# Kernel tuning notes

Measured on AMD Instinct MI355X. Metric: run time of the kernel, lower is better.

## Reference

```python
import jax, jax.numpy as jnp
import numpy as np
from jax import lax

T, B, A_DIM, Z_DIM, K_MIX, HID = 128, 256, 16, 32, 8, 128
Q_REG = 1e-3
R_REG = 1e-3


def setup_inputs() -> dict:
    key = jax.random.key(0)
    ks = jax.random.split(key, 16)
    s = 1.0 / np.sqrt(HID)
    reg = 0.9
    as_ = jax.random.normal(ks[0], (T, B, A_DIM), dtype=jnp.float32)
    mat_A_K = (1.0 - reg) * jax.random.normal(ks[1], (K_MIX, Z_DIM, Z_DIM)) + reg * jnp.eye(Z_DIM)
    mat_C_K = (1.0 - reg) * jax.random.normal(ks[2], (K_MIX, A_DIM, Z_DIM)) + reg * jnp.eye(A_DIM, Z_DIM)
    # Cholesky factors of near-identity SPD matrices (as in torch init)
    Q_L = jnp.tril(0.05 * jax.random.normal(ks[3], (Z_DIM, Z_DIM))) + jnp.eye(Z_DIM)
    R_L = jnp.tril(0.05 * jax.random.normal(ks[4], (A_DIM, A_DIM))) + jnp.eye(A_DIM)
    init_mean = jnp.zeros((Z_DIM,), dtype=jnp.float32)
    init_cov = jnp.eye(Z_DIM, dtype=jnp.float32)
    u = lambda k, shp: jax.random.uniform(k, shp, minval=-s, maxval=s, dtype=jnp.float32)
    return dict(
        as_=as_, mat_A_K=mat_A_K, mat_C_K=mat_C_K, Q_L=Q_L, R_L=R_L,
        init_mean=init_mean, init_cov=init_cov,
        W_ih0=u(ks[5], (4 * HID, A_DIM)), W_hh0=u(ks[6], (4 * HID, HID)),
        b_ih0=u(ks[7], (4 * HID,)), b_hh0=u(ks[8], (4 * HID,)),
        W_ih1=u(ks[9], (4 * HID, HID)), W_hh1=u(ks[10], (4 * HID, HID)),
        b_ih1=u(ks[11], (4 * HID,)), b_hh1=u(ks[12], (4 * HID,)),
        W_out=u(ks[13], (K_MIX, HID)), b_out=u(ks[14], (K_MIX,)),
    )


def _lstm_cell(x, h, c, W_ih, W_hh, b_ih, b_hh):
    g = x @ W_ih.T + b_ih + h @ W_hh.T + b_hh
    i, f, gg, o = jnp.split(g, 4, axis=-1)
    c2 = jax.nn.sigmoid(f) * c + jax.nn.sigmoid(i) * jnp.tanh(gg)
    h2 = jax.nn.sigmoid(o) * jnp.tanh(c2)
    return h2, c2


def reference(as_, mat_A_K, mat_C_K, Q_L, R_L, init_mean, init_cov,
              W_ih0, W_hh0, b_ih0, b_hh0, W_ih1, W_hh1, b_ih1, b_hh1,
              W_out, b_out):
    Tn, Bn, a_dim = as_.shape
    Kn, z_dim, _ = mat_A_K.shape
    Hn = W_hh0.shape[1]
    Q = Q_L @ Q_L.T + Q_REG * jnp.eye(z_dim, dtype=as_.dtype)
    R = R_L @ R_L.T + R_REG * jnp.eye(a_dim, dtype=as_.dtype)

    def weight_model(a, h0, c0, h1, c1):
        h0, c0 = _lstm_cell(a, h0, c0, W_ih0, W_hh0, b_ih0, b_hh0)
        h1, c1 = _lstm_cell(h0, h1, c1, W_ih1, W_hh1, b_ih1, b_hh1)
        w = jax.nn.softmax(h1 @ W_out.T + b_out, axis=-1)
        return w, h0, c0, h1, c1

    def step(carry, a_t):
        mean_p, cov_p, weight, h0, c0, h1, c1 = carry
        # mixture matrices for this step (weight == previous step's w_next; ones at t=0)
        mat_A = jnp.einsum('bk,kij->bij', weight, mat_A_K)
        mat_C = jnp.einsum('bk,kij->bij', weight, mat_C_K)
        # sample_control = ('mean','mean'), observation_mask=None -> a = as_[t]
        w_next, h0, c0, h1, c1 = weight_model(a_t, h0, c0, h1, c1)
        mat_A_next = jnp.einsum('bk,kij->bij', w_next, mat_A_K)
        CP = mat_C @ cov_p                                   # (B,a,z)
        S = CP @ jnp.swapaxes(mat_C, 1, 2) + R               # (B,a,a)
        K_t = cov_p @ jnp.swapaxes(mat_C, 1, 2) @ jnp.linalg.inv(S)
        mean_t = mean_p + K_t @ (a_t[..., None] - mat_C @ mean_p)
        mean_p2 = mat_A_next @ mean_t
        cov_t = cov_p - K_t @ CP
        cov_t = 0.5 * (cov_t + jnp.swapaxes(cov_t, 1, 2))
        cov_p2 = mat_A_next @ cov_t @ jnp.swapaxes(mat_A_next, 1, 2) + Q
        cov_p2 = 0.5 * (cov_p2 + jnp.swapaxes(cov_p2, 1, 2))
        new_carry = (mean_p2, cov_p2, w_next, h0, c0, h1, c1)
        outs = (mean_t, cov_t, mean_p2, cov_p2, mat_A, mat_C, a_t)
        return new_carry, outs

    init = (
        jnp.broadcast_to(init_mean[None, :, None], (Bn, z_dim, 1)),
        jnp.broadcast_to(init_cov[None], (Bn, z_dim, z_dim)),
        jnp.ones((Bn, Kn), dtype=as_.dtype),
        jnp.zeros((Bn, Hn), dtype=as_.dtype), jnp.zeros((Bn, Hn), dtype=as_.dtype),
        jnp.zeros((Bn, Hn), dtype=as_.dtype), jnp.zeros((Bn, Hn), dtype=as_.dtype),
    )
    carry, ys = lax.scan(step, init, as_)
    means, covs, next_means, next_covs, mat_As, mat_Cs, a_seq = ys
    w_fin = carry[2]
    mat_A_fin = jnp.einsum('bk,kij->bij', w_fin, mat_A_K)
    mat_C_fin = jnp.einsum('bk,kij->bij', w_fin, mat_C_K)
    mat_As = jnp.concatenate([mat_As, mat_A_fin[None]], axis=0)   # (T+1,B,z,z)
    mat_Cs = jnp.concatenate([mat_Cs, mat_C_fin[None]], axis=0)   # (T+1,B,a,z)
    a_out = a_seq[:, None]                                        # (T,1,B,a) as in torch stack
    return means, covs, next_means, next_covs, mat_As, mat_Cs, a_out
```

## Files before the change

### kernel.cpp

```cpp
#include <hip/hip_runtime.h>
#include <hip/hip_fp16.h>
#include <math.h>

#define T_STEPS 128
#define B_SZ 256
#define AD 16
#define ZD 32
#define KM 8
#define HID 128
#define G4H 512
#define NTHR 512

#define WS_WQ   0
#define WS_WI0  98304
#define WS_BS0  102400
#define WS_BS1  102912
#define WS_Q    103424
#define WS_R    104448

typedef float f32x4 __attribute__((ext_vector_type(4)));

__device__ __forceinline__ unsigned pk16(float lo, float hi) {
  unsigned a = __half_as_ushort(__float2half_rn(lo));
  unsigned b = __half_as_ushort(__float2half_rn(hi));
  return a | (b << 16);
}

__global__ void ssm_prep_kernel(const float* __restrict__ Wih0, const float* __restrict__ Whh0,
                                const float* __restrict__ Wih1, const float* __restrict__ Whh1,
                                const float* __restrict__ bih0, const float* __restrict__ bhh0,
                                const float* __restrict__ bih1, const float* __restrict__ bhh1,
                                const float* __restrict__ QL, const float* __restrict__ RL,
                                float* __restrict__ ws) {
  unsigned* wsu = (unsigned*)ws;
  int tid = blockIdx.x * blockDim.x + threadIdx.x;
  int nt = gridDim.x * blockDim.x;
  for (int j = tid; j < G4H; j += nt) {
    for (int d4 = 0; d4 < 48; ++d4) {
      for (int m = 0; m < 4; ++m) {
        int dd = (d4 & 15) * 4 + m;
        const float* src = (d4 < 16) ? Whh0 : (d4 < 32) ? Wih1 : Whh1;
        wsu[WS_WQ + (d4 * 512 + j) * 4 + m] =
            pk16(src[j * 128 + 2 * dd], src[j * 128 + 2 * dd + 1]);
      }
    }
    for (int k = 0; k < 8; ++k)
      wsu[WS_WI0 + k * 512 + j] = pk16(Wih0[j * 16 + 2 * k], Wih0[j * 16 + 2 * k + 1]);
    ws[WS_BS0 + j] = bih0[j] + bhh0[j];
    ws[WS_BS1 + j] = bih1[j] + bhh1[j];
  }
  for (int e = tid; e < ZD * ZD; e += nt) {
    int i = e >> 5, j = e & 31;
    float s = 0.f;
    for (int k = 0; k < ZD; ++k) s += QL[i * ZD + k] * QL[j * ZD + k];
    if (i == j) s += 0.001f;
    ws[WS_Q + e] = s;
  }
  for (int e = tid; e < AD * AD; e += nt) {
    int i = e >> 4, j = e & 15;
    float s = 0.f;
    for (int k = 0; k < AD; ++k) s += RL[i * AD + k] * RL[j * AD + k];
    if (i == j) s += 0.001f;
    ws[WS_R + e] = s;
  }
}

__device__ __forceinline__ float sigm(float x) { return 1.0f / (1.0f + expf(-x)); }
__device__ __forceinline__ float dotv(f32x4 a, f32x4 b) {
  return a[0] * b[0] + a[1] * b[1] + a[2] * b[2] + a[3] * b[3];
}
__device__ __forceinline__ void st_nt(float* p, float v) { __builtin_nontemporal_store(v, p); }
__device__ __forceinline__ void st_nt4(float* p, f32x4 v) {
  __builtin_nontemporal_store(v, (f32x4*)p);
}

__device__ __forceinline__ float dot2f(unsigned a, unsigned b, float c) {
#if __has_builtin(__builtin_amdgcn_fdot2)
  typedef _Float16 h2 __attribute__((ext_vector_type(2)));
  union U { unsigned u; h2 h; };
  U ua, ub; ua.u = a; ub.u = b;
  return __builtin_amdgcn_fdot2(ua.h, ub.h, c, false);
#else
  union U { unsigned u; _Float16 h[2]; };
  U ua, ub; ua.u = a; ub.u = b;
  return c + (float)ua.h[0] * (float)ub.h[0] + (float)ua.h[1] * (float)ub.h[1];
#endif
}

struct alignas(16) LS {
  unsigned ap[8];
  unsigned h0p[64];
  unsigned h1p[64];
  float g[G4H];
  float lgp[16];
};

__global__ void __launch_bounds__(NTHR, 2) ssm_lstm_kernel(
    const float* __restrict__ as_, const float* __restrict__ AK, const float* __restrict__ CK,
    const float* __restrict__ Wout, const float* __restrict__ bout,
    const float* __restrict__ ws, float* __restrict__ out) {
  __shared__ LS s;
  const int tid = threadIdx.x;
  const int b = blockIdx.x;
  const unsigned* wsu = (const unsigned*)ws;
  const uint4* Wg = (const uint4*)(wsu + WS_WQ);
  const f32x4* AK4 = (const f32x4*)AK;
  const f32x4* CK4 = (const f32x4*)CK;

  float* o_As = out + (size_t)T_STEPS * B_SZ * ZD + (size_t)T_STEPS * B_SZ * ZD * ZD +
                (size_t)T_STEPS * B_SZ * ZD + (size_t)T_STEPS * B_SZ * ZD * ZD;
  float* o_Cs = o_As + (size_t)(T_STEPS + 1) * B_SZ * ZD * ZD;
  float* o_a = o_Cs + (size_t)(T_STEPS + 1) * B_SZ * AD * ZD;

  const uint4* h0p4 = (const uint4*)s.h0p;
  const uint4* h1p4 = (const uint4*)s.h1p;
  const uint4* ap4 = (const uint4*)s.ap;

  unsigned wi0r[8];
  #pragma unroll
  for (int k = 0; k < 8; ++k) wi0r[k] = wsu[WS_WI0 + k * 512 + tid];
  const float bs0r = ws[WS_BS0 + tid];
  const float bs1r = ws[WS_BS1 + tid];
  float woutr[8];
  #pragma unroll
  for (int gi = 0; gi < KM; ++gi) woutr[gi] = (tid < HID) ? Wout[gi * HID + tid] : 0.f;
  float boutr[8];
  #pragma unroll
  for (int k = 0; k < KM; ++k) boutr[k] = bout[k];

  float c0r = 0.f, c1r = 0.f;

  if (tid < 64) { s.h0p[tid] = 0u; s.h1p[tid] = 0u; }
  if (tid < AD) {
    float v = as_[(size_t)b * AD + tid];
    ((__half*)s.ap)[tid] = __float2half_rn(v);
    st_nt(&o_a[(size_t)b * AD + tid], v);
  }
  if (tid < 256) {
    f32x4 acc = {0.f, 0.f, 0.f, 0.f};
    #pragma unroll
    for (int k = 0; k < KM; ++k) acc += AK4[k * 256 + tid];
    st_nt4(&o_As[(size_t)b * 1024 + tid * 4], acc);
  } else if (tid < 384) {
    int idx = tid - 256;
    f32x4 acc = {0.f, 0.f, 0.f, 0.f};
    #pragma unroll
    for (int k = 0; k < KM; ++k) acc += CK4[k * 128 + idx];
    st_nt4(&o_Cs[(size_t)b * 512 + idx * 4], acc);
  }
  __syncthreads();

  for (int t = 0; t < T_STEPS; ++t) {
    const size_t tb2 = (size_t)(t + 1) * B_SZ + b;

    {
      float acc = bs0r;
      #pragma unroll
      for (int k4 = 0; k4 < 2; ++k4) {
        uint4 av = ap4[k4];
        acc = dot2f(av.x, wi0r[k4 * 4 + 0], acc);
        acc = dot2f(av.y, wi0r[k4 * 4 + 1], acc);
        acc = dot2f(av.z, wi0r[k4 * 4 + 2], acc);
        acc = dot2f(av.w, wi0r[k4 * 4 + 3], acc);
      }
      #pragma unroll
      for (int d4 = 0; d4 < 16; ++d4) {
        uint4 w = Wg[d4 * 512 + tid];
        uint4 hv = h0p4[d4];
        acc = dot2f(hv.x, w.x, acc);
        acc = dot2f(hv.y, w.y, acc);
        acc = dot2f(hv.z, w.z, acc);
        acc = dot2f(hv.w, w.w, acc);
      }
      s.g[tid] = acc;
    }
    __syncthreads();

    if (tid < HID) {
      float ig = sigm(s.g[tid]);
      float fg = sigm(s.g[HID + tid]);
      float gg = tanhf(s.g[2 * HID + tid]);
      float og = sigm(s.g[3 * HID + tid]);
      c0r = fg * c0r + ig * gg;
      ((__half*)s.h0p)[tid] = __float2half_rn(og * tanhf(c0r));
    }
    __syncthreads();

    {
      float acc = bs1r;
      #pragma unroll
      for (int d4 = 0; d4 < 16; ++d4) {
        uint4 w = Wg[(16 + d4) * 512 + tid];
        uint4 hv = h0p4[d4];
        acc = dot2f(hv.x, w.x, acc);
        acc = dot2f(hv.y, w.y, acc);
        acc = dot2f(hv.z, w.z, acc);
        acc = dot2f(hv.w, w.w, acc);
      }
      #pragma unroll
      for (int d4 = 0; d4 < 16; ++d4) {
        uint4 w = Wg[(32 + d4) * 512 + tid];
        uint4 hv = h1p4[d4];
        acc = dot2f(hv.x, w.x, acc);
        acc = dot2f(hv.y, w.y, acc);
        acc = dot2f(hv.z, w.z, acc);
        acc = dot2f(hv.w, w.w, acc);
      }
      s.g[tid] = acc;
    }
    __syncthreads();

    if (tid < HID) {
      float ig = sigm(s.g[tid]);
      float fg = sigm(s.g[HID + tid]);
      float gg = tanhf(s.g[2 * HID + tid]);
      float og = sigm(s.g[3 * HID + tid]);
      c1r = fg * c1r + ig * gg;
      float h1u = og * tanhf(c1r);
      ((__half*)s.h1p)[tid] = __float2half_rn(h1u);
      int w2 = tid >> 6, lane = tid & 63;
      #pragma unroll
      for (int gi = 0; gi < KM; ++gi) {
        float p = woutr[gi] * h1u;
        #pragma unroll
        for (int m = 32; m >= 1; m >>= 1) p += __shfl_xor(p, m);
        if (lane == 0) s.lgp[w2 * KM + gi] = p;
      }
    }
    __syncthreads();

    {
      float lg[KM];
      float mx = -1e30f;
      #pragma unroll
      for (int k = 0; k < KM; ++k) {
        lg[k] = s.lgp[k] + s.lgp[KM + k] + boutr[k];
        mx = fmaxf(mx, lg[k]);
      }
      float sum = 0.f;
      #pragma unroll
      for (int k = 0; k < KM; ++k) { lg[k] = expf(lg[k] - mx); sum += lg[k]; }
      float inv = 1.0f / sum;
      #pragma unroll
      for (int k = 0; k < KM; ++k) lg[k] *= inv;
      if (tid < 256) {
        f32x4 acc = {0.f, 0.f, 0.f, 0.f};
        #pragma unroll
        for (int k = 0; k < KM; ++k) acc += lg[k] * AK4[k * 256 + tid];
        st_nt4(&o_As[tb2 * 1024 + tid * 4], acc);
      } else if (tid < 384) {
        int idx = tid - 256;
        f32x4 acc = {0.f, 0.f, 0.f, 0.f};
        #pragma unroll
        for (int k = 0; k < KM; ++k) acc += lg[k] * CK4[k * 128 + idx];
        st_nt4(&o_Cs[tb2 * 512 + idx * 4], acc);
      } else if (tid >= 448 && tid < 448 + AD && t < T_STEPS - 1) {
        int i = tid - 448;
        float v = as_[tb2 * AD + i];
        ((__half*)s.ap)[i] = __float2half_rn(v);
        st_nt(&o_a[tb2 * AD + i], v);
      }
    }
    __syncthreads();
  }
}

struct alignas(16) KS {
  float P[ZD * 36];
  float An[ZD * 36];
  float Mt[ZD * 36];
  float MtT[ZD * 36];
  float Sy[ZD * 36];
  float ACt[ZD * 36];
  float Qs[ZD * 36];
  float C[AD * 36];
  float Aug[AD * 52];
  float Kk[ZD * 20];
  float Rs[AD * AD];
  float meanp[ZD], meant[ZD], r[AD], af[AD];
};

__global__ void __launch_bounds__(256, 1) ssm_kalman_kernel(
    const float* __restrict__ as_, const float* __restrict__ initm,
    const float* __restrict__ initc, const float* __restrict__ ws,
    float* __restrict__ out) {
  __shared__ KS s;
  const int l = threadIdx.x;
  const int b = blockIdx.x;
  const int i32 = l & 31, cq = l >> 5;
  const int i16 = l & 15, j16 = l >> 4;

  float* o_means = out;
  float* o_covs = o_means + (size_t)T_STEPS * B_SZ * ZD;
  float* o_nmean = o_covs + (size_t)T_STEPS * B_SZ * ZD * ZD;
  float* o_ncovs = o_nmean + (size_t)T_STEPS * B_SZ * ZD;
  const float* o_As = o_ncovs + (size_t)T_STEPS * B_SZ * ZD * ZD;
  const float* o_Cs = o_As + (size_t)(T_STEPS + 1) * B_SZ * ZD * ZD;

  f32x4* P4 = (f32x4*)s.P;
  f32x4* An4 = (f32x4*)s.An;
  f32x4* Mt4 = (f32x4*)s.Mt;
  f32x4* MtT4 = (f32x4*)s.MtT;
  f32x4* Sy4 = (f32x4*)s.Sy;
  f32x4* ACt4 = (f32x4*)s.ACt;
  f32x4* Q4 = (f32x4*)s.Qs;
  f32x4* C4 = (f32x4*)s.C;
  f32x4* Aug4 = (f32x4*)s.Aug;
  f32x4* Kk4 = (f32x4*)s.Kk;
  f32x4* af4 = (f32x4*)s.af;
  const f32x4* r4 = (const f32x4*)s.r;
  const f32x4* meanp4 = (const f32x4*)s.meanp;
  const f32x4* meant4 = (const f32x4*)s.meant;

  #pragma unroll
  for (int q = 0; q < 4; ++q) {
    int e = q * 256 + l;
    s.P[(e >> 5) * 36 + (e & 31)] = initc[e];
    s.Qs[(e >> 5) * 36 + (e & 31)] = ws[WS_Q + e];
  }
  s.Rs[l] = ws[WS_R + l];
  if (l < ZD) s.meanp[l] = initm[l];
  {
    const f32x4* gc = (const f32x4*)&o_Cs[(size_t)b * 512];
    if (l < 128) C4[(l >> 3) * 9 + (l & 7)] = gc[l];
    const f32x4* ga = (const f32x4*)&o_As[((size_t)B_SZ + b) * 1024];
    An4[(l >> 3) * 9 + (l & 7)] = ga[l];
    if (l < 4) af4[l] = ((const f32x4*)&as_[(size_t)b * AD])[l];
  }
  __syncthreads();

  for (int t = 0; t < T_STEPS; ++t) {
    const size_t tb = (size_t)t * B_SZ + b;
    const bool pf = (t < T_STEPS - 1);

    f32x4 pfC = {0, 0, 0, 0};
    f32x4 pfA = {0, 0, 0, 0};
    f32x4 pfa = {0, 0, 0, 0};
    if (pf) {
      if (l >= 128) pfC = ((const f32x4*)&o_Cs[(tb + B_SZ) * 512])[l - 128];
      pfA = ((const f32x4*)&o_As[(tb + 2 * B_SZ) * 1024])[l];
      if (l < 4) pfa = ((const f32x4*)&as_[(tb + B_SZ) * AD])[l];
    }

    {
      float a0 = 0.f, a1 = 0.f;
      #pragma unroll
      for (int k4 = 0; k4 < 8; ++k4) {
        f32x4 cr = C4[i16 * 9 + k4];
        a0 += dotv(cr, P4[j16 * 9 + k4]);
        a1 += dotv(cr, P4[(j16 + 16) * 9 + k4]);
      }
      s.Aug[i16 * 52 + AD + j16] = a0;
      s.Aug[i16 * 52 + AD + j16 + 16] = a1;
    }
    __syncthreads();

    {
      float acc = s.Rs[i16 * AD + j16];
      #pragma unroll
      for (int k4 = 0; k4 < 8; ++k4)
        acc += dotv(Aug4[i16 * 13 + 4 + k4], C4[j16 * 9 + k4]);
      s.Aug[i16 * 52 + j16] = acc;
      if (l >= 240) {
        int ii = l - 240;
        float rr = s.af[ii];
        #pragma unroll
        for (int k4 = 0; k4 < 8; ++k4) rr -= dotv(C4[ii * 9 + k4], meanp4[k4]);
        s.r[ii] = rr;
      }
    }
    __syncthreads();

    if (l < 64) {
      const int lc = (l < 48) ? l : 47;
      float col[16];
      #pragma unroll
      for (int i = 0; i < AD; ++i) col[i] = s.Aug[i * 52 + lc];
      #pragma unroll
      for (int j = 0; j < AD; ++j) {
        float pd = __shfl(col[j], j);
        float pinv = 1.0f / pd;
        float oldj = col[j];
        #pragma unroll
        for (int i = 0; i < AD; ++i) {
          if (i == j) continue;
          float fi = __shfl(col[i], j);
          col[i] = fmaf(-(fi * pinv), oldj, col[i]);
        }
        col[j] = oldj * pinv;
      }
      if (l >= AD && l < AD + ZD) {
        int rr = l - AD;
        f32x4 v0 = {col[0], col[1], col[2], col[3]};
        f32x4 v1 = {col[4], col[5], col[6], col[7]};
        f32x4 v2 = {col[8], col[9], col[10], col[11]};
        f32x4 v3 = {col[12], col[13], col[14], col[15]};
        Kk4[rr * 5 + 0] = v0;
        Kk4[rr * 5 + 1] = v1;
        Kk4[rr * 5 + 2] = v2;
        Kk4[rr * 5 + 3] = v3;
      }
    } else if (pf && l >= 128) {
      int idx = l - 128;
      C4[(idx >> 3) * 9 + (idx & 7)] = pfC;
    }
    __syncthreads();

    {
      f32x4 acc = {0.f, 0.f, 0.f, 0.f};
      #pragma unroll
      for (int k4 = 0; k4 < 4; ++k4) {
        f32x4 kv = Kk4[i32 * 5 + k4];
        #pragma unroll
        for (int kk = 0; kk < 4; ++kk) {
          f32x4 cpk = Aug4[(4 * k4 + kk) * 13 + 4 + cq];
          acc += kv[kk] * cpk;
        }
      }
      f32x4 mv = P4[i32 * 9 + cq] - acc;
      Mt4[i32 * 9 + cq] = mv;
      #pragma unroll
      for (int jj = 0; jj < 4; ++jj) s.MtT[(4 * cq + jj) * 36 + i32] = mv[jj];
    }
    __syncthreads();

    {
      f32x4 sv = 0.5f * (Mt4[i32 * 9 + cq] + MtT4[i32 * 9 + cq]);
      Sy4[i32 * 9 + cq] = sv;
      st_nt4(&o_covs[tb * 1024 + i32 * 32 + cq * 4], sv);
      if (l < ZD) {
        float acc = s.meanp[l];
        #pragma unroll
        for (int m = 0; m < 4; ++m) acc += dotv(Kk4[l * 5 + m], r4[m]);
        s.meant[l] = acc;
        st_nt(&o_means[tb * ZD + l], acc);
      }
    }
    __syncthreads();

    {
      float c0 = 0.f, c1 = 0.f, c2 = 0.f, c3 = 0.f;
      #pragma unroll
      for (int k4 = 0; k4 < 8; ++k4) {
        f32x4 an = An4[i32 * 9 + k4];
        c0 += dotv(an, Sy4[(4 * cq + 0) * 9 + k4]);
        c1 += dotv(an, Sy4[(4 * cq + 1) * 9 + k4]);
        c2 += dotv(an, Sy4[(4 * cq + 2) * 9 + k4]);
        c3 += dotv(an, Sy4[(4 * cq + 3) * 9 + k4]);
      }
      f32x4 v = {c0, c1, c2, c3};
      ACt4[i32 * 9 + cq] = v;
    }
    __syncthreads();

    {
      if (l < ZD) {
        float acc = 0.f;
        #pragma unroll
        for (int k4 = 0; k4 < 8; ++k4) acc += dotv(An4[l * 9 + k4], meant4[k4]);
        s.meanp[l] = acc;
        st_nt(&o_nmean[tb * ZD + l], acc);
      }
      float c0 = 0.f, c1 = 0.f, c2 = 0.f, c3 = 0.f;
      #pragma unroll
      for (int k4 = 0; k4 < 8; ++k4) {
        f32x4 ac = ACt4[i32 * 9 + k4];
        c0 += dotv(ac, An4[(4 * cq + 0) * 9 + k4]);
        c1 += dotv(ac, An4[(4 * cq + 1) * 9 + k4]);
        c2 += dotv(ac, An4[(4 * cq + 2) * 9 + k4]);
        c3 += dotv(ac, An4[(4 * cq + 3) * 9 + k4]);
      }
      f32x4 mv = {c0, c1, c2, c3};
      Mt4[i32 * 9 + cq] = mv;
      #pragma unroll
      for (int jj = 0; jj < 4; ++jj) s.MtT[(4 * cq + jj) * 36 + i32] = mv[jj];
    }
    __syncthreads();

    {
      f32x4 pv = 0.5f * (Mt4[i32 * 9 + cq] + MtT4[i32 * 9 + cq]) + Q4[i32 * 9 + cq];
      P4[i32 * 9 + cq] = pv;
      st_nt4(&o_ncovs[tb * 1024 + i32 * 32 + cq * 4], pv);
    }
    __syncthreads();

    if (pf) {
      An4[(l >> 3) * 9 + (l & 7)] = pfA;
      if (l < 4) af4[l] = pfa;
    }
    __syncthreads();
  }
}

extern "C" void kernel_launch(void* const* d_in, const int* in_sizes, int n_in,
                              void* d_out, int out_size, void* d_ws, size_t ws_size,
                              hipStream_t stream) {
  const float* as_ = (const float*)d_in[0];
  const float* AK = (const float*)d_in[1];
  const float* CK = (const float*)d_in[2];
  const float* QL = (const float*)d_in[3];
  const float* RL = (const float*)d_in[4];
  const float* initm = (const float*)d_in[5];
  const float* initc = (const float*)d_in[6];
  const float* Wih0 = (const float*)d_in[7];
  const float* Whh0 = (const float*)d_in[8];
  const float* bih0 = (const float*)d_in[9];
  const float* bhh0 = (const float*)d_in[10];
  const float* Wih1 = (const float*)d_in[11];
  const float* Whh1 = (const float*)d_in[12];
  const float* bih1 = (const float*)d_in[13];
  const float* bhh1 = (const float*)d_in[14];
  const float* Wout = (const float*)d_in[15];
  const float* bout = (const float*)d_in[16];
  float* ws = (float*)d_ws;
  float* out = (float*)d_out;

  ssm_prep_kernel<<<16, 256, 0, stream>>>(Wih0, Whh0, Wih1, Whh1, bih0, bhh0, bih1, bhh1,
                                          QL, RL, ws);
  ssm_lstm_kernel<<<B_SZ, NTHR, 0, stream>>>(as_, AK, CK, Wout, bout, ws, out);
  ssm_kalman_kernel<<<B_SZ, 256, 0, stream>>>(as_, initm, initc, ws, out);
}
```

Baseline: 1.588 ms.

## Process two batch rows per LSTM block and merge Kalman output stores into one phase

The LSTM kernel now handles two batch elements per workgroup, so each weight fragment loaded from global memory feeds two dot-product accumulators. This halves weight traffic per row and halves the grid to 128 blocks. The catch is that fewer blocks run on the GPU, which has 256 CUs. The Kalman kernel also defers its means, covs and next-mean stores to the final phase and folds the prefetch update into it, removing one barrier per step.

```diff
diff --git a/kernel.cpp b/kernel.cpp
--- a/kernel.cpp
+++ b/kernel.cpp
@@ -9,7 +9,6 @@
 #define KM 8
 #define HID 128
 #define G4H 512
-#define NTHR 512
 
 #define WS_WQ   0
 #define WS_WI0  98304
@@ -88,20 +87,20 @@
 }
 
 struct alignas(16) LS {
-  unsigned ap[8];
-  unsigned h0p[64];
-  unsigned h1p[64];
-  float g[G4H];
-  float lgp[16];
+  unsigned ap[2][8];
+  unsigned h0p[2][64];
+  unsigned h1p[2][64];
+  float g[2][G4H];
+  float lgp[4][KM];
 };
 
-__global__ void __launch_bounds__(NTHR, 2) ssm_lstm_kernel(
+__global__ void __launch_bounds__(512, 2) ssm_lstm_kernel(
     const float* __restrict__ as_, const float* __restrict__ AK, const float* __restrict__ CK,
     const float* __restrict__ Wout, const float* __restrict__ bout,
     const float* __restrict__ ws, float* __restrict__ out) {
   __shared__ LS s;
   const int tid = threadIdx.x;
-  const int b = blockIdx.x;
+  const int b0 = blockIdx.x * 2;
   const unsigned* wsu = (const unsigned*)ws;
   const uint4* Wg = (const uint4*)(wsu + WS_WQ);
   const f32x4* AK4 = (const f32x4*)AK;
@@ -112,9 +111,12 @@
   float* o_Cs = o_As + (size_t)(T_STEPS + 1) * B_SZ * ZD * ZD;
   float* o_a = o_Cs + (size_t)(T_STEPS + 1) * B_SZ * AD * ZD;
 
-  const uint4* h0p4 = (const uint4*)s.h0p;
-  const uint4* h1p4 = (const uint4*)s.h1p;
-  const uint4* ap4 = (const uint4*)s.ap;
+  const uint4* ap40 = (const uint4*)s.ap[0];
+  const uint4* ap41 = (const uint4*)s.ap[1];
+  const uint4* h0p40 = (const uint4*)s.h0p[0];
+  const uint4* h0p41 = (const uint4*)s.h0p[1];
+  const uint4* h1p40 = (const uint4*)s.h1p[0];
+  const uint4* h1p41 = (const uint4*)s.h1p[1];
 
   unsigned wi0r[8];
   #pragma unroll
@@ -123,142 +125,162 @@
   const float bs1r = ws[WS_BS1 + tid];
   float woutr[8];
   #pragma unroll
-  for (int gi = 0; gi < KM; ++gi) woutr[gi] = (tid < HID) ? Wout[gi * HID + tid] : 0.f;
+  for (int gi = 0; gi < KM; ++gi)
+    woutr[gi] = (tid < 256) ? Wout[gi * HID + (tid & 127)] : 0.f;
   float boutr[8];
   #pragma unroll
   for (int k = 0; k < KM; ++k) boutr[k] = bout[k];
 
   float c0r = 0.f, c1r = 0.f;
 
-  if (tid < 64) { s.h0p[tid] = 0u; s.h1p[tid] = 0u; }
-  if (tid < AD) {
-    float v = as_[(size_t)b * AD + tid];
-    ((__half*)s.ap)[tid] = __float2half_rn(v);
-    st_nt(&o_a[(size_t)b * AD + tid], v);
-  }
-  if (tid < 256) {
+  if (tid < 128) { ((unsigned*)s.h0p)[tid] = 0u; ((unsigned*)s.h1p)[tid] = 0u; }
+  if (tid < 32) {
+    int bq = tid >> 4, i = tid & 15;
+    float v = as_[(size_t)(b0 + bq) * AD + i];
+    ((__half*)s.ap[bq])[i] = __float2half_rn(v);
+    st_nt(&o_a[(size_t)(b0 + bq) * AD + i], v);
+  }
+  {
+    int bq = tid >> 8, e = tid & 255;
     f32x4 acc = {0.f, 0.f, 0.f, 0.f};
     #pragma unroll
-    for (int k = 0; k < KM; ++k) acc += AK4[k * 256 + tid];
-    st_nt4(&o_As[(size_t)b * 1024 + tid * 4], acc);
-  } else if (tid < 384) {
-    int idx = tid - 256;
+    for (int k = 0; k < KM; ++k) acc += AK4[k * 256 + e];
+    st_nt4(&o_As[((size_t)(b0 + bq)) * 1024 + e * 4], acc);
+  }
+  if (tid < 256) {
+    int bq = tid >> 7, e = tid & 127;
     f32x4 acc = {0.f, 0.f, 0.f, 0.f};
     #pragma unroll
-    for (int k = 0; k < KM; ++k) acc += CK4[k * 128 + idx];
-    st_nt4(&o_Cs[(size_t)b * 512 + idx * 4], acc);
+    for (int k = 0; k < KM; ++k) acc += CK4[k * 128 + e];
+    st_nt4(&o_Cs[((size_t)(b0 + bq)) * 512 + e * 4], acc);
   }
   __syncthreads();
 
   for (int t = 0; t < T_STEPS; ++t) {
-    const size_t tb2 = (size_t)(t + 1) * B_SZ + b;
-
-    {
-      float acc = bs0r;
+    {
+      float a0 = bs0r, a1 = bs0r;
       #pragma unroll
       for (int k4 = 0; k4 < 2; ++k4) {
-        uint4 av = ap4[k4];
-        acc = dot2f(av.x, wi0r[k4 * 4 + 0], acc);
-        acc = dot2f(av.y, wi0r[k4 * 4 + 1], acc);
-        acc = dot2f(av.z, wi0r[k4 * 4 + 2], acc);
-        acc = dot2f(av.w, wi0r[k4 * 4 + 3], acc);
+        uint4 av0 = ap40[k4], av1 = ap41[k4];
+        a0 = dot2f(av0.x, wi0r[k4 * 4 + 0], a0); a1 = dot2f(av1.x, wi0r[k4 * 4 + 0], a1);
+        a0 = dot2f(av0.y, wi0r[k4 * 4 + 1], a0); a1 = dot2f(av1.y, wi0r[k4 * 4 + 1], a1);
+        a0 = dot2f(av0.z, wi0r[k4 * 4 + 2], a0); a1 = dot2f(av1.z, wi0r[k4 * 4 + 2], a1);
+        a0 = dot2f(av0.w, wi0r[k4 * 4 + 3], a0); a1 = dot2f(av1.w, wi0r[k4 * 4 + 3], a1);
       }
       #pragma unroll
       for (int d4 = 0; d4 < 16; ++d4) {
         uint4 w = Wg[d4 * 512 + tid];
-        uint4 hv = h0p4[d4];
-        acc = dot2f(hv.x, w.x, acc);
-        acc = dot2f(hv.y, w.y, acc);
-        acc = dot2f(hv.z, w.z, acc);
-        acc = dot2f(hv.w, w.w, acc);
-      }
-      s.g[tid] = acc;
-    }
-    __syncthreads();
-
-    if (tid < HID) {
-      float ig = sigm(s.g[tid]);
-      float fg = sigm(s.g[HID + tid]);
-      float gg = tanhf(s.g[2 * HID + tid]);
-      float og = sigm(s.g[3 * HID + tid]);
+        uint4 h0 = h0p40[d4], h1 = h0p41[d4];
+        a0 = dot2f(h0.x, w.x, a0); a1 = dot2f(h1.x, w.x, a1);
+        a0 = dot2f(h0.y, w.y, a0); a1 = dot2f(h1.y, w.y, a1);
+        a0 = dot2f(h0.z, w.z, a0); a1 = dot2f(h1.z, w.z, a1);
+        a0 = dot2f(h0.w, w.w, a0); a1 = dot2f(h1.w, w.w, a1);
+      }
+      s.g[0][tid] = a0;
+      s.g[1][tid] = a1;
+    }
+    __syncthreads();
+
+    if (tid < 256) {
+      int ub = tid >> 7, u = tid & 127;
+      float ig = sigm(s.g[ub][u]);
+      float fg = sigm(s.g[ub][HID + u]);
+      float gg = tanhf(s.g[ub][2 * HID + u]);
+      float og = sigm(s.g[ub][3 * HID + u]);
       c0r = fg * c0r + ig * gg;
-      ((__half*)s.h0p)[tid] = __float2half_rn(og * tanhf(c0r));
-    }
-    __syncthreads();
-
-    {
-      float acc = bs1r;
+      ((__half*)s.h0p[ub])[u] = __float2half_rn(og * tanhf(c0r));
+    }
+    __syncthreads();
+
+    {
+      float a0 = bs1r, a1 = bs1r;
       #pragma unroll
       for (int d4 = 0; d4 < 16; ++d4) {
         uint4 w = Wg[(16 + d4) * 512 + tid];
-        uint4 hv = h0p4[d4];
-        acc = dot2f(hv.x, w.x, acc);
-        acc = dot2f(hv.y, w.y, acc);
-        acc = dot2f(hv.z, w.z, acc);
-        acc = dot2f(hv.w, w.w, acc);
+        uint4 h0 = h0p40[d4], h1 = h0p41[d4];
+        a0 = dot2f(h0.x, w.x, a0); a1 = dot2f(h1.x, w.x, a1);
+        a0 = dot2f(h0.y, w.y, a0); a1 = dot2f(h1.y, w.y, a1);
+        a0 = dot2f(h0.z, w.z, a0); a1 = dot2f(h1.z, w.z, a1);
+        a0 = dot2f(h0.w, w.w, a0); a1 = dot2f(h1.w, w.w, a1);
       }
       #pragma unroll
       for (int d4 = 0; d4 < 16; ++d4) {
         uint4 w = Wg[(32 + d4) * 512 + tid];
-        uint4 hv = h1p4[d4];
-        acc = dot2f(hv.x, w.x, acc);
-        acc = dot2f(hv.y, w.y, acc);
-        acc = dot2f(hv.z, w.z, acc);
-        acc = dot2f(hv.w, w.w, acc);
-      }
-      s.g[tid] = acc;
-    }
-    __syncthreads();
-
-    if (tid < HID) {
-      float ig = sigm(s.g[tid]);
-      float fg = sigm(s.g[HID + tid]);
-      float gg = tanhf(s.g[2 * HID + tid]);
-      float og = sigm(s.g[3 * HID + tid]);
+        uint4 h0 = h1p40[d4], h1 = h1p41[d4];
+        a0 = dot2f(h0.x, w.x, a0); a1 = dot2f(h1.x, w.x, a1);
+        a0 = dot2f(h0.y, w.y, a0); a1 = dot2f(h1.y, w.y, a1);
+        a0 = dot2f(h0.z, w.z, a0); a1 = dot2f(h1.z, w.z, a1);
+        a0 = dot2f(h0.w, w.w, a0); a1 = dot2f(h1.w, w.w, a1);
+      }
+      s.g[0][tid] = a0;
+      s.g[1][tid] = a1;
+    }
+    __syncthreads();
+
+    if (tid < 256) {
+      int ub = tid >> 7, u = tid & 127;
+      float ig = sigm(s.g[ub][u]);
+      float fg = sigm(s.g[ub][HID + u]);
+      float gg = tanhf(s.g[ub][2 * HID + u]);
+      float og = sigm(s.g[ub][3 * HID + u]);
       c1r = fg * c1r + ig * gg;
       float h1u = og * tanhf(c1r);
-      ((__half*)s.h1p)[tid] = __float2half_rn(h1u);
+      ((__half*)s.h1p[ub])[u] = __float2half_rn(h1u);
       int w2 = tid >> 6, lane = tid & 63;
       #pragma unroll
       for (int gi = 0; gi < KM; ++gi) {
         float p = woutr[gi] * h1u;
         #pragma unroll
         for (int m = 32; m >= 1; m >>= 1) p += __shfl_xor(p, m);
-        if (lane == 0) s.lgp[w2 * KM + gi] = p;
-      }
-    }
-    __syncthreads();
-
-    {
-      float lg[KM];
-      float mx = -1e30f;
+        if (lane == 0) s.lgp[w2][gi] = p;
+      }
+    }
+    __syncthreads();
+
+    {
+      float lg0[KM], lg1[KM];
+      float mx0 = -1e30f, mx1 = -1e30f;
       #pragma unroll
       for (int k = 0; k < KM; ++k) {
-        lg[k] = s.lgp[k] + s.lgp[KM + k] + boutr[k];
-        mx = fmaxf(mx, lg[k]);
-      }
-      float sum = 0.f;
-      #pragma unroll
-      for (int k = 0; k < KM; ++k) { lg[k] = expf(lg[k] - mx); sum += lg[k]; }
-      float inv = 1.0f / sum;
-      #pragma unroll
-      for (int k = 0; k < KM; ++k) lg[k] *= inv;
+        lg0[k] = s.lgp[0][k] + s.lgp[1][k] + boutr[k];
+        lg1[k] = s.lgp[2][k] + s.lgp[3][k] + boutr[k];
+        mx0 = fmaxf(mx0, lg0[k]);
+        mx1 = fmaxf(mx1, lg1[k]);
+      }
+      float s0 = 0.f, s1 = 0.f;
+      #pragma unroll
+      for (int k = 0; k < KM; ++k) {
+        lg0[k] = expf(lg0[k] - mx0); s0 += lg0[k];
+        lg1[k] = expf(lg1[k] - mx1); s1 += lg1[k];
+      }
+      float i0 = 1.0f / s0, i1 = 1.0f / s1;
+      #pragma unroll
+      for (int k = 0; k < KM; ++k) { lg0[k] *= i0; lg1[k] *= i1; }
+
+      {
+        int bq = tid >> 8, e = tid & 255;
+        f32x4 acc = {0.f, 0.f, 0.f, 0.f};
+        #pragma unroll
+        for (int k = 0; k < KM; ++k) {
+          float wk = bq ? lg1[k] : lg0[k];
+          acc += wk * AK4[k * 256 + e];
+        }
+        st_nt4(&o_As[((size_t)(t + 1) * B_SZ + b0 + bq) * 1024 + e * 4], acc);
+      }
       if (tid < 256) {
+        int bq = tid >> 7, e = tid & 127;
         f32x4 acc = {0.f, 0.f, 0.f, 0.f};
         #pragma unroll
-        for (int k = 0; k < KM; ++k) acc += lg[k] * AK4[k * 256 + tid];
-        st_nt4(&o_As[tb2 * 1024 + tid * 4], acc);
-      } else if (tid < 384) {
-        int idx = tid - 256;
-        f32x4 acc = {0.f, 0.f, 0.f, 0.f};
-        #pragma unroll
-        for (int k = 0; k < KM; ++k) acc += lg[k] * CK4[k * 128 + idx];
-        st_nt4(&o_Cs[tb2 * 512 + idx * 4], acc);
-      } else if (tid >= 448 && tid < 448 + AD && t < T_STEPS - 1) {
-        int i = tid - 448;
-        float v = as_[tb2 * AD + i];
-        ((__half*)s.ap)[i] = __float2half_rn(v);
-        st_nt(&o_a[tb2 * AD + i], v);
+        for (int k = 0; k < KM; ++k) {
+          float wk = bq ? lg1[k] : lg0[k];
+          acc += wk * CK4[k * 128 + e];
+        }
+        st_nt4(&o_Cs[((size_t)(t + 1) * B_SZ + b0 + bq) * 512 + e * 4], acc);
+      } else if (tid >= 480 && t < T_STEPS - 1) {
+        int idx = tid - 480, bq = idx >> 4, i = idx & 15;
+        float v = as_[((size_t)(t + 1) * B_SZ + b0 + bq) * AD + i];
+        ((__half*)s.ap[bq])[i] = __float2half_rn(v);
+        st_nt(&o_a[((size_t)(t + 1) * B_SZ + b0 + bq) * AD + i], v);
       }
     }
     __syncthreads();
@@ -342,6 +364,9 @@
       if (l < 4) pfa = ((const f32x4*)&as_[(tb + B_SZ) * AD])[l];
     }
 
+    float meant_r = 0.f, nmean_r = 0.f;
+    f32x4 covs_r = {0, 0, 0, 0};
+
     {
       float a0 = 0.f, a1 = 0.f;
       #pragma unroll
@@ -425,15 +450,14 @@
     __syncthreads();
 
     {
-      f32x4 sv = 0.5f * (Mt4[i32 * 9 + cq] + MtT4[i32 * 9 + cq]);
-      Sy4[i32 * 9 + cq] = sv;
-      st_nt4(&o_covs[tb * 1024 + i32 * 32 + cq * 4], sv);
+      covs_r = 0.5f * (Mt4[i32 * 9 + cq] + MtT4[i32 * 9 + cq]);
+      Sy4[i32 * 9 + cq] = covs_r;
       if (l < ZD) {
         float acc = s.meanp[l];
         #pragma unroll
         for (int m = 0; m < 4; ++m) acc += dotv(Kk4[l * 5 + m], r4[m]);
         s.meant[l] = acc;
-        st_nt(&o_means[tb * ZD + l], acc);
+        meant_r = acc;
       }
     }
     __syncthreads();
@@ -459,7 +483,7 @@
         #pragma unroll
         for (int k4 = 0; k4 < 8; ++k4) acc += dotv(An4[l * 9 + k4], meant4[k4]);
         s.meanp[l] = acc;
-        st_nt(&o_nmean[tb * ZD + l], acc);
+        nmean_r = acc;
       }
       float c0 = 0.f, c1 = 0.f, c2 = 0.f, c3 = 0.f;
       #pragma unroll
@@ -481,12 +505,15 @@
       f32x4 pv = 0.5f * (Mt4[i32 * 9 + cq] + MtT4[i32 * 9 + cq]) + Q4[i32 * 9 + cq];
       P4[i32 * 9 + cq] = pv;
       st_nt4(&o_ncovs[tb * 1024 + i32 * 32 + cq * 4], pv);
-    }
-    __syncthreads();
-
-    if (pf) {
-      An4[(l >> 3) * 9 + (l & 7)] = pfA;
-      if (l < 4) af4[l] = pfa;
+      st_nt4(&o_covs[tb * 1024 + i32 * 32 + cq * 4], covs_r);
+      if (l < ZD) {
+        st_nt(&o_means[tb * ZD + l], meant_r);
+        st_nt(&o_nmean[tb * ZD + l], nmean_r);
+      }
+      if (pf) {
+        An4[(l >> 3) * 9 + (l & 7)] = pfA;
+        if (l < 4) af4[l] = pfa;
+      }
     }
     __syncthreads();
   }
@@ -517,6 +544,6 @@
 
   ssm_prep_kernel<<<16, 256, 0, stream>>>(Wih0, Whh0, Wih1, Whh1, bih0, bhh0, bih1, bhh1,
                                           QL, RL, ws);
-  ssm_lstm_kernel<<<B_SZ, NTHR, 0, stream>>>(as_, AK, CK, Wout, bout, ws, out);
+  ssm_lstm_kernel<<<B_SZ / 2, 512, 0, stream>>>(as_, AK, CK, Wout, bout, ws, out);
   ssm_kalman_kernel<<<B_SZ, 256, 0, stream>>>(as_, initm, initc, ws, out);
 }
```

Result: slower. 2.320 ms (+46.1%).
